# Kernel optimization log

Hardware: AMD Instinct MI355X
Metric: run time of the kernel (lower is better)

The kernel has to match this reference:

```python
import jax, jax.numpy as jnp
import numpy as np

HIDDEN = 2048
N_HEADS = 32
N_KV = 4
HEAD_DIM = 128
EPS = 1e-6
THETA = 1e6
B, S = 2, 2048


def setup_inputs() -> dict:
    key = jax.random.key(0)
    k1, k2, k3 = jax.random.split(key, 3)
    hidden_states = jax.random.normal(k1, (B, S, HIDDEN), dtype=jnp.float32)
    positions = jnp.broadcast_to(jnp.arange(S, dtype=jnp.int32), (B, S))
    w_qkv = jax.random.normal(k2, ((N_HEADS + 2 * N_KV) * HEAD_DIM, HIDDEN), dtype=jnp.float32) * 0.02
    w_o = jax.random.normal(k3, (HIDDEN, N_HEADS * HEAD_DIM), dtype=jnp.float32) * 0.02
    q_norm_w = jnp.ones((HEAD_DIM,), dtype=jnp.float32)
    k_norm_w = jnp.ones((HEAD_DIM,), dtype=jnp.float32)
    return {"hidden_states": hidden_states, "positions": positions,
            "w_qkv": w_qkv, "w_o": w_o, "q_norm_w": q_norm_w, "k_norm_w": k_norm_w}


def _rms_norm(x, w):
    # x: [..., HEAD_DIM]
    var = jnp.mean(x * x, axis=-1, keepdims=True)
    return x * jax.lax.rsqrt(var + EPS) * w


def _rope(x, positions):
    # NEOX-style rotary. x: [B,S,H,D], positions: [B,S]
    half = HEAD_DIM // 2
    inv_freq = 1.0 / (THETA ** (jnp.arange(0, half, dtype=jnp.float32) / half))
    ang = positions.astype(jnp.float32)[..., None] * inv_freq  # [B,S,half]
    cos = jnp.cos(ang)[:, :, None, :]
    sin = jnp.sin(ang)[:, :, None, :]
    x1, x2 = x[..., :half], x[..., half:]
    return jnp.concatenate([x1 * cos - x2 * sin, x2 * cos + x1 * sin], axis=-1)


def reference(hidden_states, positions, w_qkv, w_o, q_norm_w, k_norm_w):
    q_size = N_HEADS * HEAD_DIM
    kv_size = N_KV * HEAD_DIM
    qkv = jnp.einsum('bsh,oh->bso', hidden_states, w_qkv)
    q = qkv[..., :q_size].reshape(B, S, N_HEADS, HEAD_DIM)
    k = qkv[..., q_size:q_size + kv_size].reshape(B, S, N_KV, HEAD_DIM)
    v = qkv[..., q_size + kv_size:].reshape(B, S, N_KV, HEAD_DIM)
    # per-head RMSNorm then RoPE
    q = _rope(_rms_norm(q, q_norm_w), positions)
    k = _rope(_rms_norm(k, k_norm_w), positions)
    rep = N_HEADS // N_KV
    k = jnp.repeat(k, rep, axis=2)
    v = jnp.repeat(v, rep, axis=2)
    scale = HEAD_DIM ** -0.5
    scores = jnp.einsum('bqhd,bkhd->bhqk', q, k) * scale
    causal = jnp.tril(jnp.ones((S, S), dtype=bool))
    scores = jnp.where(causal, scores, jnp.finfo(scores.dtype).min)
    probs = jax.nn.softmax(scores, axis=-1)
    attn = jnp.einsum('bhqk,bkhd->bqhd', probs, v).reshape(B, S, N_HEADS * HEAD_DIM)
    return jnp.einsum('bsa,ha->bsh', attn, w_o)
```

## Files before the change

### kernel.cpp

```cpp
#include <hip/hip_runtime.h>
#include <cstdint>

#define SEQ 2048
#define BATCH 2
#define NTOK 4096
#define HID 2048
#define NH 32
#define NKV 4
#define HD 128
#define QKV_O 5120

typedef __attribute__((ext_vector_type(8))) short short8;
typedef __attribute__((ext_vector_type(8))) unsigned short u16x8;
typedef __attribute__((ext_vector_type(4))) unsigned short u16x4;
typedef __attribute__((ext_vector_type(4))) float f32x4;

__device__ __forceinline__ float bf2f(unsigned short u) {
  union { unsigned int i; float f; } v; v.i = ((unsigned int)u) << 16; return v.f;
}
__device__ __forceinline__ unsigned short f2bf(float f) {
  union { float f; unsigned int i; } v; v.f = f;
  unsigned int r = v.i + 0x7FFFu + ((v.i >> 16) & 1u);
  return (unsigned short)(r >> 16);
}

__device__ __forceinline__ void load_lds16(const void* g, void* l) {
  __builtin_amdgcn_global_load_lds((const __attribute__((address_space(1))) unsigned int*)g,
                                   (__attribute__((address_space(3))) unsigned int*)l, 16, 0, 0);
}

__global__ __launch_bounds__(256) void convert_to_bf16(const float* __restrict__ src,
                                                       unsigned short* __restrict__ dst,
                                                       int n4) {
  int i = blockIdx.x * blockDim.x + threadIdx.x;
  int stride = gridDim.x * blockDim.x;
  for (; i < n4; i += stride) {
    f32x4 v = *(const f32x4*)(src + 4 * (size_t)i);
    u16x4 o;
    o.x = f2bf(v.x); o.y = f2bf(v.y); o.z = f2bf(v.z); o.w = f2bf(v.w);
    *(u16x4*)(dst + 4 * (size_t)i) = o;
  }
}

__global__ __launch_bounds__(256) void reduce_add(float* __restrict__ out,
                                                  const float* __restrict__ part, int n4) {
  int i = blockIdx.x * blockDim.x + threadIdx.x;
  int stride = gridDim.x * blockDim.x;
  for (; i < n4; i += stride) {
    f32x4 a = *(const f32x4*)(out + 4 * (size_t)i);
    f32x4 b = *(const f32x4*)(part + 4 * (size_t)i);
    a.x += b.x; a.y += b.y; a.z += b.z; a.w += b.w;
    *(f32x4*)(out + 4 * (size_t)i) = a;
  }
}

template <bool OUT_F32, bool SPLIT>
__global__ __launch_bounds__(512, 2) void gemm256(
    const unsigned short* __restrict__ A, const unsigned short* __restrict__ B,
    void* __restrict__ C0, void* __restrict__ C1,
    int lda, int ldb, int ldc, int Kloop) {
  __shared__ alignas(16) unsigned short As[2][256 * 64];
  __shared__ alignas(16) unsigned short Bs[2][256 * 64];

  const int t = threadIdx.x;
  const int lane = t & 63, w = t >> 6;
  const int fr = lane & 15, g = lane >> 4;
  const int wm = w >> 2, wn = w & 3;
  const size_t m0 = (size_t)blockIdx.y * 256;
  const size_t n0 = (size_t)blockIdx.x * 256;
  const int kbase = SPLIT ? (int)blockIdx.z * Kloop : 0;
  void* Cv = (SPLIT && blockIdx.z) ? C1 : C0;

  const int srow = w * 8 + (lane >> 3);
  const int sch = (lane & 7) ^ ((lane >> 3) & 7);
  const unsigned short* gA[4];
  const unsigned short* gB[4];
#pragma unroll
  for (int i = 0; i < 4; i++) {
    gA[i] = A + (m0 + i * 64 + srow) * (size_t)lda + kbase + sch * 8;
    gB[i] = B + (n0 + i * 64 + srow) * (size_t)ldb + kbase + sch * 8;
  }

  auto stage = [&](int k0, int bi) {
#pragma unroll
    for (int i = 0; i < 4; i++) {
      load_lds16(gA[i] + k0, &As[bi][(i * 512 + w * 64) * 8]);
      load_lds16(gB[i] + k0, &Bs[bi][(i * 512 + w * 64) * 8]);
    }
  };

  f32x4 acc[8][4] = {};
  stage(0, 0);

  const int nk = Kloop / 64;
  for (int kt = 0; kt < nk; kt++) {
    const int cur = kt & 1;
    asm volatile("s_waitcnt vmcnt(0)" ::: "memory");
    __builtin_amdgcn_s_barrier();
    __builtin_amdgcn_sched_barrier(0);
    if (kt + 1 < nk) stage((kt + 1) * 64, cur ^ 1);

    const unsigned short* Ac = As[cur];
    const unsigned short* Bc = Bs[cur];

    short8 bfr[4][2];
#pragma unroll
    for (int nf = 0; nf < 4; nf++) {
      const int row = wn * 64 + nf * 16 + fr;
#pragma unroll
      for (int s = 0; s < 2; s++)
        bfr[nf][s] = *(const short8*)&Bc[row * 64 + (((s * 4 + g) ^ (fr & 7)) * 8)];
    }
    __builtin_amdgcn_s_setprio(1);
#pragma unroll
    for (int mf = 0; mf < 8; mf++) {
      const int row = wm * 128 + mf * 16 + fr;
      short8 af0 = *(const short8*)&Ac[row * 64 + (((0 + g) ^ (fr & 7)) * 8)];
      short8 af1 = *(const short8*)&Ac[row * 64 + (((4 + g) ^ (fr & 7)) * 8)];
#pragma unroll
      for (int nf = 0; nf < 4; nf++) {
        acc[mf][nf] = __builtin_amdgcn_mfma_f32_16x16x32_bf16(af0, bfr[nf][0], acc[mf][nf], 0, 0, 0);
        acc[mf][nf] = __builtin_amdgcn_mfma_f32_16x16x32_bf16(af1, bfr[nf][1], acc[mf][nf], 0, 0, 0);
      }
    }
    __builtin_amdgcn_s_setprio(0);
  }

#pragma unroll
  for (int mf = 0; mf < 8; mf++)
#pragma unroll
    for (int nf = 0; nf < 4; nf++) {
      size_t row = m0 + wm * 128 + mf * 16 + g * 4;
      size_t col = n0 + wn * 64 + nf * 16 + fr;
#pragma unroll
      for (int r = 0; r < 4; r++) {
        if (OUT_F32) ((float*)Cv)[(row + r) * ldc + col] = acc[mf][nf][r];
        else ((unsigned short*)Cv)[(row + r) * ldc + col] = f2bf(acc[mf][nf][r]);
      }
    }
}

__global__ __launch_bounds__(64) void rope_tab(const int* __restrict__ pos,
                                               float2* __restrict__ tab) {
  const int tok = blockIdx.x;
  const int j = threadIdx.x;
  float p = (float)pos[tok];
  float inv_freq = expf((float)j * (-13.815510557964274f / 64.0f));
  float ang = p * inv_freq;
  float2 cs; cs.x = cosf(ang); cs.y = sinf(ang);
  tab[tok * 64 + j] = cs;
}

__global__ __launch_bounds__(256) void normrope(
    unsigned short* __restrict__ qkv, const float2* __restrict__ tab,
    const unsigned short* __restrict__ qw, const unsigned short* __restrict__ kw) {
  const int wv   = threadIdx.x >> 6;
  const int lane = threadIdx.x & 63;
  const int h    = blockIdx.x * 4 + wv;
  const int tok  = blockIdx.z * SEQ + blockIdx.y;

  const unsigned short* w = (h < NH) ? qw : kw;
  const size_t src = (size_t)tok * QKV_O + (size_t)h * HD;

  float x1 = bf2f(qkv[src + lane]);
  float x2 = bf2f(qkv[src + lane + 64]);
  float ss = x1 * x1 + x2 * x2;
#pragma unroll
  for (int off = 32; off; off >>= 1) ss += __shfl_xor(ss, off);
  float r = rsqrtf(ss * (1.0f / 128.0f) + 1e-6f);
  float n1 = x1 * r * bf2f(w[lane]);
  float n2 = x2 * r * bf2f(w[lane + 64]);

  float2 cs = tab[tok * 64 + lane];
  qkv[src + lane]      = f2bf(n1 * cs.x - n2 * cs.y);
  qkv[src + lane + 64] = f2bf(n2 * cs.x + n1 * cs.y);
}

__global__ __launch_bounds__(256) void transpose_v(const unsigned short* __restrict__ qkv,
                                                   unsigned short* __restrict__ vt) {
  __shared__ alignas(16) unsigned short Vs[64][136];
  const int k0 = blockIdx.x * 64, kvh = blockIdx.y, b = blockIdx.z;
  const int t = threadIdx.x;
  const int voff = (NH + NKV) * HD + kvh * HD;
  {
    const int row = t >> 2, cb = (t & 3) * 8;
    const size_t gb = (size_t)(b * SEQ + k0 + row) * QKV_O + voff;
#pragma unroll
    for (int r = 0; r < 4; r++)
      *(uint4*)&Vs[row][cb + 32 * r] = *(const uint4*)&qkv[gb + cb + 32 * r];
  }
  __syncthreads();
  const int d = t >> 1, half = t & 1;
  const size_t ob = ((size_t)((b * NKV + kvh) * HD + d)) * SEQ + k0 + half * 32;
#pragma unroll
  for (int i = 0; i < 4; i++) {
    u16x8 vv;
#pragma unroll
    for (int j = 0; j < 8; j++) vv[j] = Vs[half * 32 + i * 8 + j][d];
    *(u16x8*)&vt[ob + i * 8] = vv;
  }
}

__global__ __launch_bounds__(512, 4) void flash_mfma(unsigned short* __restrict__ qkv,
                                                     const unsigned short* __restrict__ vt) {
  __shared__ alignas(16) unsigned short Kbuf[2][64 * 128];
  __shared__ alignas(16) unsigned short Vbuf[2][128 * 64];
  __shared__ alignas(16) unsigned short Ps[8][16 * 64];

  const int p = (int)blockIdx.x;
  const int h = blockIdx.y, b = blockIdx.z;
  const int t = threadIdx.x;
  const int lane = t & 63, w = t >> 6;
  const int c = lane & 15, g = lane >> 4;
  const int kvh = h >> 3;
  const int koff = NH * HD + kvh * HD;
  const float scale = 0.08838834764831845f;
  const int swz = c & 7;
  const int nqt = SEQ / 128;

  const int rK0 = t >> 4,         jK0 = (t & 15) ^ (rK0 & 15);
  const int rK1 = (t + 512) >> 4, jK1 = ((t + 512) & 15) ^ (rK1 & 15);
  const int dV0 = t >> 3,         jV0 = (t & 7) ^ (dV0 & 7);
  const int dV1 = (t + 512) >> 3, jV1 = ((t + 512) & 7) ^ (dV1 & 7);
  const unsigned short* gK0 = qkv + (size_t)(b * SEQ + rK0) * QKV_O + koff + jK0 * 8;
  const unsigned short* gK1 = qkv + (size_t)(b * SEQ + rK1) * QKV_O + koff + jK1 * 8;
  const unsigned short* gV0 = vt + ((size_t)(b * NKV + kvh) * HD + dV0) * SEQ + jV0 * 8;
  const unsigned short* gV1 = vt + ((size_t)(b * NKV + kvh) * HD + dV1) * SEQ + jV1 * 8;

  auto stage = [&](int k0s, int bi) {
    load_lds16(gK0 + (size_t)k0s * QKV_O, &Kbuf[bi][(w * 64) * 8]);
    load_lds16(gK1 + (size_t)k0s * QKV_O, &Kbuf[bi][(w * 64 + 512) * 8]);
    load_lds16(gV0 + k0s, &Vbuf[bi][(w * 64) * 8]);
    load_lds16(gV1 + k0s, &Vbuf[bi][(w * 64 + 512) * 8]);
  };

  for (int job = 0; job < 2; job++) {
    const int qt = job == 0 ? (nqt - 1 - p) : p;
    const int q0 = qt * 128;
    const int nkt = 2 * qt + 2;

    stage(0, 0);

    short8 qf[4];
    {
      const size_t qr = (size_t)(b * SEQ + q0 + w * 16 + c) * QKV_O + (size_t)h * HD;
#pragma unroll
      for (int ks = 0; ks < 4; ks++)
        qf[ks] = *(const short8*)&qkv[qr + ks * 32 + g * 8];
    }

    f32x4 O[8] = {};
    float m_i = -1e30f, l_i = 0.0f;

    for (int kt = 0; kt < nkt; kt++) {
      const int cur = kt & 1;
      asm volatile("s_waitcnt vmcnt(0)" ::: "memory");
      __builtin_amdgcn_s_barrier();
      __builtin_amdgcn_sched_barrier(0);
      if (kt + 1 < nkt) stage((kt + 1) * 64, cur ^ 1);

      const unsigned short* Kc = Kbuf[cur];
      const unsigned short* Vc = Vbuf[cur];

      f32x4 sc[4];
#pragma unroll
      for (int mt = 0; mt < 4; mt++) sc[mt] = (f32x4){0.f, 0.f, 0.f, 0.f};
      __builtin_amdgcn_s_setprio(1);
#pragma unroll
      for (int ks = 0; ks < 4; ks++) {
#pragma unroll
        for (int mt = 0; mt < 4; mt++) {
          short8 kf = *(const short8*)&Kc[(mt * 16 + c) * 128 + (((ks * 4 + g) ^ c) * 8)];
          sc[mt] = __builtin_amdgcn_mfma_f32_16x16x32_bf16(kf, qf[ks], sc[mt], 0, 0, 0);
        }
      }
      __builtin_amdgcn_s_setprio(0);

      const int k0 = kt * 64;
      const int qrow = q0 + w * 16 + c;
      const bool need_mask = (k0 + 63 > q0 + w * 16);
      float mx = -3.0e38f;
#pragma unroll
      for (int mt = 0; mt < 4; mt++)
#pragma unroll
        for (int r = 0; r < 4; r++) {
          float s = sc[mt][r];
          if (need_mask && (k0 + mt * 16 + g * 4 + r > qrow)) s = -3.0e38f;
          sc[mt][r] = s;
          mx = fmaxf(mx, s);
        }
      mx = fmaxf(mx, __shfl_xor(mx, 16));
      mx = fmaxf(mx, __shfl_xor(mx, 32));
      float mxs = mx * scale;

      if (!__all(mxs - m_i <= 8.0f)) {
        float m_new = fmaxf(m_i, mxs);
        float alpha = __expf(m_i - m_new);
        f32x4 a4;
#pragma unroll
        for (int r = 0; r < 4; r++) a4[r] = __shfl(alpha, g * 4 + r);
#pragma unroll
        for (int nt = 0; nt < 8; nt++)
#pragma unroll
          for (int r = 0; r < 4; r++) O[nt][r] *= a4[r];
        l_i *= alpha;
        m_i = m_new;
      }

      float psum = 0.0f;
#pragma unroll
      for (int mt = 0; mt < 4; mt++) {
        u16x4 p4;
#pragma unroll
        for (int r = 0; r < 4; r++) {
          float pv = __expf(__builtin_fmaf(sc[mt][r], scale, -m_i));
          psum += pv;
          p4[r] = f2bf(pv);
        }
        *(u16x4*)&Ps[w][c * 64 + (((mt * 2 + (g >> 1)) ^ swz) * 8) + (g & 1) * 4] = p4;
      }
      psum += __shfl_xor(psum, 16);
      psum += __shfl_xor(psum, 32);
      l_i += psum;

      __builtin_amdgcn_s_setprio(1);
#pragma unroll
      for (int ks = 0; ks < 2; ks++) {
        short8 pf = *(const short8*)&Ps[w][c * 64 + (((ks * 4 + g) ^ swz) * 8)];
#pragma unroll
        for (int nt = 0; nt < 8; nt++) {
          short8 vf = *(const short8*)&Vc[(nt * 16 + c) * 64 + (((ks * 4 + g) ^ swz) * 8)];
          O[nt] = __builtin_amdgcn_mfma_f32_16x16x32_bf16(pf, vf, O[nt], 0, 0, 0);
        }
      }
      __builtin_amdgcn_s_setprio(0);
    }

    f32x4 l4;
#pragma unroll
    for (int r = 0; r < 4; r++) l4[r] = __shfl(l_i, g * 4 + r);
    f32x4 li;
#pragma unroll
    for (int r = 0; r < 4; r++) li[r] = 1.0f / l4[r];
#pragma unroll
    for (int nt = 0; nt < 8; nt++)
#pragma unroll
      for (int r = 0; r < 4; r++) {
        size_t addr = (size_t)(b * SEQ + q0 + w * 16 + g * 4 + r) * QKV_O + h * HD + nt * 16 + c;
        qkv[addr] = f2bf(O[nt][r] * li[r]);
      }
  }
}

extern "C" void kernel_launch(void* const* d_in, const int* in_sizes, int n_in,
                              void* d_out, int out_size, void* d_ws, size_t ws_size,
                              hipStream_t stream) {
  const float* hidden_f = (const float*)d_in[0];
  const int* positions  = (const int*)d_in[1];
  const float* wqkv_f   = (const float*)d_in[2];
  const float* wo_f     = (const float*)d_in[3];
  const float* qn_f     = (const float*)d_in[4];
  const float* kn_f     = (const float*)d_in[5];
  float* out            = (float*)d_out;

  char* ws = (char*)d_ws;
  unsigned short* hidden_c = (unsigned short*)ws;
  unsigned short* wqkv_c   = (unsigned short*)(ws + 16777216);
  unsigned short* wo_c     = (unsigned short*)(ws + 37748736);
  unsigned short* qn_c     = (unsigned short*)(ws + 54525952);
  unsigned short* kn_c     = (unsigned short*)(ws + 54526208);
  unsigned short* qkv      = (unsigned short*)(ws + 54526464);
  unsigned short* vt_g     = (unsigned short*)(ws + 96469504);
  float2* rtab             = (float2*)ws;
  float* p0                = (float*)ws;

  convert_to_bf16<<<1024, 256, 0, stream>>>(hidden_f, hidden_c, NTOK * HID / 4);
  convert_to_bf16<<<1024, 256, 0, stream>>>(wqkv_f, wqkv_c, QKV_O * HID / 4);
  convert_to_bf16<<<1024, 256, 0, stream>>>(wo_f, wo_c, HID * NH * HD / 4);
  convert_to_bf16<<<1, 32, 0, stream>>>(qn_f, qn_c, HD / 4);
  convert_to_bf16<<<1, 32, 0, stream>>>(kn_f, kn_c, HD / 4);

  gemm256<false, false><<<dim3(QKV_O / 256, NTOK / 256), 512, 0, stream>>>(
      hidden_c, wqkv_c, qkv, qkv, HID, HID, QKV_O, HID);
  rope_tab<<<NTOK, 64, 0, stream>>>(positions, rtab);
  normrope<<<dim3((NH + NKV) / 4, SEQ, BATCH), 256, 0, stream>>>(qkv, rtab, qn_c, kn_c);
  transpose_v<<<dim3(SEQ / 64, NKV, BATCH), 256, 0, stream>>>(qkv, vt_g);
  flash_mfma<<<dim3(SEQ / 256, NH, BATCH), 512, 0, stream>>>(qkv, vt_g);
  gemm256<true, true><<<dim3(HID / 256, NTOK / 256, 2), 512, 0, stream>>>(
      qkv, wo_c, p0, out, QKV_O, NH * HD, HID, NH * HD / 2);
  reduce_add<<<2048, 256, 0, stream>>>(out, p0, NTOK * HID / 4);
}
```

Baseline: 480.0 us.

## Split QKV GEMM into 256-tile Q part and 128-tile KV kernel; pack bf16 cvt

The QKV projection is split in two. The 256x256-tile GEMM now covers only the Q columns (4096), and a new simpler 128x128-tile bf16 GEMM covers the 1024 K/V columns, so tile counts divide evenly and wave quantisation on the GPU improves. Separately, the flash kernel now converts probabilities to bf16 with the hardware v_cvt_pk_bf16_f32 instruction instead of software rounding. The new GEMM has no double buffering, and the extra launch adds overhead.

```diff
diff --git a/kernel.cpp b/kernel.cpp
--- a/kernel.cpp
+++ b/kernel.cpp
@@ -140,6 +140,72 @@
     }
 }
 
+template <bool OUT_F32>
+__global__ __launch_bounds__(256) void gemm_bt_bf16(
+    const unsigned short* __restrict__ A, const unsigned short* __restrict__ B,
+    void* __restrict__ Cv, int lda, int ldb, int ldc, int K) {
+  __shared__ alignas(16) unsigned short As[128 * 32];
+  __shared__ alignas(16) unsigned short Bs[128 * 32];
+
+  const int t    = threadIdx.x;
+  const int lane = t & 63;
+  const int w    = t >> 6;
+  const int wm   = (w >> 1) * 64;
+  const int wn   = (w & 1) * 64;
+  const size_t m0 = (size_t)blockIdx.y * 128;
+  const size_t n0 = (size_t)blockIdx.x * 128;
+
+  f32x4 acc[4][4] = {};
+
+  const int srow = w * 32 + (lane >> 2);
+  const int scol = (lane & 3) * 8;
+  const unsigned short* gA0 = &A[(m0 + srow) * (size_t)lda + scol];
+  const unsigned short* gA1 = gA0 + 16 * (size_t)lda;
+  const unsigned short* gB0 = &B[(n0 + srow) * (size_t)ldb + scol];
+  const unsigned short* gB1 = gB0 + 16 * (size_t)ldb;
+  unsigned short* lA0 = &As[(w * 32) * 32];
+  unsigned short* lA1 = &As[(w * 32 + 16) * 32];
+  unsigned short* lB0 = &Bs[(w * 32) * 32];
+  unsigned short* lB1 = &Bs[(w * 32 + 16) * 32];
+
+  const int fr = lane & 15;
+  const int kb = (lane >> 4) * 8;
+
+  for (int k0 = 0; k0 < K; k0 += 32) {
+    load_lds16(gA0 + k0, lA0);
+    load_lds16(gA1 + k0, lA1);
+    load_lds16(gB0 + k0, lB0);
+    load_lds16(gB1 + k0, lB1);
+    __syncthreads();
+    short8 af[4], bf[4];
+#pragma unroll
+    for (int mt = 0; mt < 4; mt++) af[mt] = *(const short8*)&As[(wm + mt * 16 + fr) * 32 + kb];
+#pragma unroll
+    for (int nt = 0; nt < 4; nt++) bf[nt] = *(const short8*)&Bs[(wn + nt * 16 + fr) * 32 + kb];
+#pragma unroll
+    for (int mt = 0; mt < 4; mt++)
+#pragma unroll
+      for (int nt = 0; nt < 4; nt++)
+        acc[mt][nt] = __builtin_amdgcn_mfma_f32_16x16x32_bf16(af[mt], bf[nt], acc[mt][nt], 0, 0, 0);
+    __syncthreads();
+  }
+
+  const int r4 = (lane >> 4) * 4;
+  const int cc = lane & 15;
+#pragma unroll
+  for (int mt = 0; mt < 4; mt++)
+#pragma unroll
+    for (int nt = 0; nt < 4; nt++) {
+      size_t row = m0 + wm + mt * 16 + r4;
+      size_t col = n0 + wn + nt * 16 + cc;
+#pragma unroll
+      for (int r = 0; r < 4; r++) {
+        if (OUT_F32) ((float*)Cv)[(row + r) * ldc + col] = acc[mt][nt][r];
+        else ((unsigned short*)Cv)[(row + r) * ldc + col] = f2bf(acc[mt][nt][r]);
+      }
+    }
+}
+
 __global__ __launch_bounds__(64) void rope_tab(const int* __restrict__ pos,
                                                float2* __restrict__ tab) {
   const int tok = blockIdx.x;
@@ -310,14 +376,17 @@
       float psum = 0.0f;
 #pragma unroll
       for (int mt = 0; mt < 4; mt++) {
-        u16x4 p4;
+        float pv[4];
 #pragma unroll
         for (int r = 0; r < 4; r++) {
-          float pv = __expf(__builtin_fmaf(sc[mt][r], scale, -m_i));
-          psum += pv;
-          p4[r] = f2bf(pv);
+          pv[r] = __expf(__builtin_fmaf(sc[mt][r], scale, -m_i));
+          psum += pv[r];
         }
-        *(u16x4*)&Ps[w][c * 64 + (((mt * 2 + (g >> 1)) ^ swz) * 8) + (g & 1) * 4] = p4;
+        unsigned int pk0, pk1;
+        asm("v_cvt_pk_bf16_f32 %0, %1, %2" : "=v"(pk0) : "v"(pv[0]), "v"(pv[1]));
+        asm("v_cvt_pk_bf16_f32 %0, %1, %2" : "=v"(pk1) : "v"(pv[2]), "v"(pv[3]));
+        uint2 pk; pk.x = pk0; pk.y = pk1;
+        *(uint2*)&Ps[w][c * 64 + (((mt * 2 + (g >> 1)) ^ swz) * 8) + (g & 1) * 4] = pk;
       }
       psum += __shfl_xor(psum, 16);
       psum += __shfl_xor(psum, 32);
@@ -380,8 +449,10 @@
   convert_to_bf16<<<1, 32, 0, stream>>>(qn_f, qn_c, HD / 4);
   convert_to_bf16<<<1, 32, 0, stream>>>(kn_f, kn_c, HD / 4);
 
-  gemm256<false, false><<<dim3(QKV_O / 256, NTOK / 256), 512, 0, stream>>>(
+  gemm256<false, false><<<dim3(NH * HD / 256, NTOK / 256), 512, 0, stream>>>(
       hidden_c, wqkv_c, qkv, qkv, HID, HID, QKV_O, HID);
+  gemm_bt_bf16<false><<<dim3(2 * NKV * HD / 128, NTOK / 128), 256, 0, stream>>>(
+      hidden_c, wqkv_c + (size_t)(NH * HD) * HID, qkv + NH * HD, HID, HID, QKV_O, HID);
   rope_tab<<<NTOK, 64, 0, stream>>>(positions, rtab);
   normrope<<<dim3((NH + NKV) / 4, SEQ, BATCH), 256, 0, stream>>>(qkv, rtab, qn_c, kn_c);
   transpose_v<<<dim3(SEQ / 64, NKV, BATCH), 256, 0, stream>>>(qkv, vt_g);
```

Result: faster. 468.0 us (-2.5%).
